# Kernel optimization log

Measured on AMD Instinct MI355X. Metric: run time of the kernel, lower is better.

Reference implementation:

```python
import jax, jax.numpy as jnp
import numpy as np

N_NODES = 50000
N_EDGES = 800000
D = 128


def _gcn_layer(x, src, dst, deg_inv_sqrt, W, b, n_nodes):
    # GCNConv: X' = D^{-1/2} (A + I) D^{-1/2} X W + b   (PyG default, self-loops added)
    h = x @ W  # [N, D]
    norm = deg_inv_sqrt[src] * deg_inv_sqrt[dst]  # [E+N]
    msgs = h[src] * norm[:, None]  # [E+N, D] gather + scale
    out = jax.ops.segment_sum(msgs, dst, num_segments=n_nodes)  # scatter-add
    return out + b


def setup_inputs() -> dict:
    key = jax.random.key(0)
    k1, k2, k3, k4 = jax.random.split(key, 4)
    x = jax.random.normal(k1, (N_NODES, D), dtype=jnp.float32)
    edge_index = jax.random.randint(k2, (2, N_EDGES), 0, N_NODES, dtype=jnp.int64)
    scale = 1.0 / np.sqrt(D)
    W1 = jax.random.normal(k3, (D, D), dtype=jnp.float32) * scale
    b1 = jnp.zeros((D,), dtype=jnp.float32)
    W2 = jax.random.normal(k4, (D, D), dtype=jnp.float32) * scale
    b2 = jnp.zeros((D,), dtype=jnp.float32)
    return {"x": x, "edge_index": edge_index, "W1": W1, "b1": b1, "W2": W2, "b2": b2}


def reference(x, edge_index, W1, b1, W2, b2):
    n_nodes = x.shape[0]
    # add self-loops once (same graph both layers)
    loop = jnp.arange(n_nodes, dtype=edge_index.dtype)
    src = jnp.concatenate([edge_index[0], loop])
    dst = jnp.concatenate([edge_index[1], loop])
    deg = jax.ops.segment_sum(jnp.ones_like(dst, dtype=x.dtype), dst, num_segments=n_nodes)
    deg_inv_sqrt = jnp.where(deg > 0, jax.lax.rsqrt(deg), 0.0)

    h = _gcn_layer(x, src, dst, deg_inv_sqrt, W1, b1, n_nodes)
    h = jax.nn.relu(h)
    h = _gcn_layer(h, src, dst, deg_inv_sqrt, W2, b2, n_nodes)
    h = jax.nn.relu(h)
    return h
```

## Files before the change

kernel.cpp:

```cpp
#include <hip/hip_runtime.h>

#define N_NODES 50000
#define N_EDGES 800000
#define D 128
#define NB 392
#define CHUNK 2048
#define NBKT 391
#define LHM (NBKT * NB)
#define NSB ((LHM + 255) / 256)
#define GB ((N_NODES + 127) / 128)

typedef unsigned int uint32;
typedef unsigned short ushort;
typedef __attribute__((ext_vector_type(8))) short s8v;
typedef __attribute__((ext_vector_type(4))) float f4v;

__device__ __forceinline__ ushort f2bf(float f) {
    unsigned u = __float_as_uint(f);
    u += 0x7FFFu + ((u >> 16) & 1u);
    return (ushort)(u >> 16);
}
__device__ __forceinline__ float bf_lo(uint32 u) { return __uint_as_float(u << 16); }
__device__ __forceinline__ float bf_hi(uint32 u) { return __uint_as_float(u & 0xFFFF0000u); }

__device__ __forceinline__ int block_incl_scan(int v, int t) {
    int lane = t & 63, wv = t >> 6;
    int incl = v;
    #pragma unroll
    for (int off = 1; off < 64; off <<= 1) {
        int u = __shfl_up(incl, off, 64);
        if (lane >= off) incl += u;
    }
    __shared__ int wsums[4];
    if (lane == 63) wsums[wv] = incl;
    __syncthreads();
    int add = 0;
    if (wv > 0) add += wsums[0];
    if (wv > 1) add += wsums[1];
    if (wv > 2) add += wsums[2];
    return incl + add;
}

__global__ __launch_bounds__(256) void phaseA_kernel(const int* __restrict__ dst,
                                                     int* __restrict__ histM,
                                                     const float* __restrict__ W1,
                                                     const float* __restrict__ W2,
                                                     ushort* __restrict__ W1t,
                                                     ushort* __restrict__ W2t) {
    int t = threadIdx.x, blk = blockIdx.x;
    if (blk >= NB) {
        const float* W = (blk - NB) ? W2 : W1;
        ushort* Wt = (blk - NB) ? W2t : W1t;
        #pragma unroll
        for (int it = 0; it < 16; it++) {
            int fid = t + it * 256;
            int k = fid >> 5;
            int n0 = (fid & 31) * 4;
            float4 w = ((const float4*)W)[fid];
            Wt[(n0 + 0) * D + k] = f2bf(w.x);
            Wt[(n0 + 1) * D + k] = f2bf(w.y);
            Wt[(n0 + 2) * D + k] = f2bf(w.z);
            Wt[(n0 + 3) * D + k] = f2bf(w.w);
        }
        return;
    }
    __shared__ int lc[NBKT];
    for (int i = t; i < NBKT; i += 256) lc[i] = 0;
    __syncthreads();
    int e0 = blk * CHUNK;
    #pragma unroll
    for (int j = 0; j < 8; j++) {
        int e = e0 + t + j * 256;
        if (e < N_EDGES) atomicAdd(&lc[dst[e] >> 7], 1);
    }
    __syncthreads();
    for (int i = t; i < NBKT; i += 256)
        histM[i * NB + blk] = lc[i];
}

__global__ __launch_bounds__(256) void scan1g(const int* __restrict__ in,
                                              int* __restrict__ out,
                                              int* __restrict__ bsum) {
    int t = threadIdx.x, blk = blockIdx.x;
    int i = blk * 256 + t;
    int v = (i < LHM) ? in[i] : 0;
    int incl = block_incl_scan(v, t);
    if (i < LHM) out[i] = incl - v;
    if (t == 255) bsum[blk] = incl;
}

__global__ __launch_bounds__(256) void scan23g(int* __restrict__ out,
                                               const int* __restrict__ bsum) {
    int t = threadIdx.x, blk = blockIdx.x;
    int local = 0;
    for (int i = t; i < blk; i += 256) local += bsum[i];
    int lane = t & 63, wv = t >> 6;
    #pragma unroll
    for (int off = 32; off > 0; off >>= 1) local += __shfl_down(local, off, 64);
    __shared__ int ws[4];
    if (lane == 0) ws[wv] = local;
    __syncthreads();
    int boff = ws[0] + ws[1] + ws[2] + ws[3];
    int i = blk * 256 + t;
    if (i < LHM) out[i] += boff;
}

__global__ __launch_bounds__(256) void phaseC_kernel(const int* __restrict__ src,
                                                     const int* __restrict__ dst,
                                                     const int* __restrict__ base,
                                                     uint32* __restrict__ edgeTmp) {
    __shared__ int cur[NBKT];
    int t = threadIdx.x, blk = blockIdx.x;
    for (int i = t; i < NBKT; i += 256) cur[i] = base[i * NB + blk];
    __syncthreads();
    int e0 = blk * CHUNK;
    #pragma unroll
    for (int j = 0; j < 8; j++) {
        int e = e0 + t + j * 256;
        if (e < N_EDGES) {
            uint32 s = (uint32)src[e], d = (uint32)dst[e];
            int p = atomicAdd(&cur[d >> 7], 1);
            edgeTmp[p] = (s << 16) | d;
        }
    }
}

__global__ __launch_bounds__(256) void phaseD_kernel(const uint32* __restrict__ edgeTmp,
                                                     const int* __restrict__ base,
                                                     int* __restrict__ rowstart,
                                                     float* __restrict__ dis,
                                                     ushort* __restrict__ e16) {
    __shared__ int cnt[128];
    __shared__ int cur[128];
    int t = threadIdx.x, b = blockIdx.x;
    int beg = base[b * NB];
    int end = (b == NBKT - 1) ? N_EDGES : base[(b + 1) * NB];
    if (t < 128) cnt[t] = 0;
    __syncthreads();
    for (int p = beg + t; p < end; p += 256)
        atomicAdd(&cnt[edgeTmp[p] & 127], 1);
    __syncthreads();
    int c = (t < 128) ? cnt[t] : 0;
    int incl = block_incl_scan(c, t);
    int excl = incl - c;
    int node = b * 128 + t;
    if (t < 128) {
        if (node <= N_NODES) rowstart[node] = beg + excl;
        if (node < N_NODES) dis[node] = rsqrtf((float)(c + 1));
        cur[t] = excl;
    }
    __syncthreads();
    for (int p = beg + t; p < end; p += 256) {
        uint32 u = edgeTmp[p];
        int r = atomicAdd(&cur[u & 127], 1);
        e16[beg + r] = (ushort)(u >> 16);
    }
}

template<bool BF16IN>
__global__ __launch_bounds__(256) void gemm_mfma(const void* __restrict__ Xv,
                                                 const ushort* __restrict__ Wt,
                                                 const float* __restrict__ dis,
                                                 ushort* __restrict__ Hb) {
    __shared__ ushort Cs[128 * 136];
    int t = threadIdx.x;
    int wv = t >> 6, lane = t & 63;
    int q = lane >> 4, m = lane & 15;
    int rbase = blockIdx.x * 128 + wv * 32;
    f4v zero = {0.f, 0.f, 0.f, 0.f};
    f4v acc[2][8];
    #pragma unroll
    for (int mt = 0; mt < 2; mt++)
        #pragma unroll
        for (int n = 0; n < 8; n++) acc[mt][n] = zero;

    #pragma unroll
    for (int kt = 0; kt < 4; kt++) {
        int k0 = kt * 32 + q * 8;
        s8v a[2];
        #pragma unroll
        for (int mt = 0; mt < 2; mt++) {
            int row = rbase + mt * 16 + m;
            if (row >= N_NODES) row = N_NODES - 1;
            if (BF16IN) {
                const ushort* xp = (const ushort*)Xv + (size_t)row * D + k0;
                a[mt] = *(const s8v*)xp;
            } else {
                const float* xp = (const float*)Xv + (size_t)row * D + k0;
                float4 u0 = *(const float4*)xp;
                float4 u1 = *(const float4*)(xp + 4);
                s8v av;
                av[0] = (short)f2bf(u0.x); av[1] = (short)f2bf(u0.y);
                av[2] = (short)f2bf(u0.z); av[3] = (short)f2bf(u0.w);
                av[4] = (short)f2bf(u1.x); av[5] = (short)f2bf(u1.y);
                av[6] = (short)f2bf(u1.z); av[7] = (short)f2bf(u1.w);
                a[mt] = av;
            }
        }
        #pragma unroll
        for (int n = 0; n < 8; n++) {
            s8v b = *(const s8v*)(Wt + (size_t)(n * 16 + m) * D + k0);
            acc[0][n] = __builtin_amdgcn_mfma_f32_16x16x32_bf16(a[0], b, acc[0][n], 0, 0, 0);
            acc[1][n] = __builtin_amdgcn_mfma_f32_16x16x32_bf16(a[1], b, acc[1][n], 0, 0, 0);
        }
    }
    float disv[2][4];
    #pragma unroll
    for (int mt = 0; mt < 2; mt++)
        #pragma unroll
        for (int r = 0; r < 4; r++) {
            int row = rbase + mt * 16 + q * 4 + r;
            if (row >= N_NODES) row = N_NODES - 1;
            disv[mt][r] = dis[row];
        }
    #pragma unroll
    for (int mt = 0; mt < 2; mt++)
        #pragma unroll
        for (int n = 0; n < 8; n++)
            #pragma unroll
            for (int r = 0; r < 4; r++) {
                int row = wv * 32 + mt * 16 + q * 4 + r;
                Cs[row * 136 + n * 16 + m] = f2bf(acc[mt][n][r] * disv[mt][r]);
            }
    __syncthreads();
    int gbase = blockIdx.x * 128;
    #pragma unroll
    for (int it = 0; it < 8; it++) {
        int cid = t + it * 256;
        int row = cid >> 4, off = (cid & 15) * 8;
        int grow = gbase + row;
        if (grow < N_NODES) {
            s8v v = *(const s8v*)(Cs + row * 136 + off);
            *(s8v*)(Hb + (size_t)grow * D + off) = v;
        }
    }
}

__device__ __forceinline__ void acc8(float* a, uint4 v) {
    a[0] += bf_lo(v.x); a[1] += bf_hi(v.x);
    a[2] += bf_lo(v.y); a[3] += bf_hi(v.y);
    a[4] += bf_lo(v.z); a[5] += bf_hi(v.z);
    a[6] += bf_lo(v.w); a[7] += bf_hi(v.w);
}

template<bool BF16OUT>
__global__ __launch_bounds__(256) void aggr_kernel(const uint4* __restrict__ Hb4,
                                                   const float* __restrict__ dis,
                                                   const int* __restrict__ rowstart,
                                                   const ushort* __restrict__ e16,
                                                   const float* __restrict__ bias,
                                                   void* __restrict__ Hout) {
    int t = threadIdx.x;
    int li = t & 15;
    int n = blockIdx.x * 16 + (t >> 4);
    float dn = dis[n];
    float a[8];
    {
        uint4 sv = Hb4[(size_t)n * 16 + li];
        a[0] = bf_lo(sv.x); a[1] = bf_hi(sv.x);
        a[2] = bf_lo(sv.y); a[3] = bf_hi(sv.y);
        a[4] = bf_lo(sv.z); a[5] = bf_hi(sv.z);
        a[6] = bf_lo(sv.w); a[7] = bf_hi(sv.w);
    }
    int beg = rowstart[n], end = rowstart[n + 1];
    int p = beg;
    for (; p + 7 < end; p += 8) {
        int s[8];
        #pragma unroll
        for (int j = 0; j < 8; j++) s[j] = e16[p + j];
        uint4 v[8];
        #pragma unroll
        for (int j = 0; j < 8; j++) v[j] = Hb4[(size_t)s[j] * 16 + li];
        #pragma unroll
        for (int j = 0; j < 8; j++) acc8(a, v[j]);
    }
    for (; p + 3 < end; p += 4) {
        int s0 = e16[p + 0], s1 = e16[p + 1], s2 = e16[p + 2], s3 = e16[p + 3];
        uint4 v0 = Hb4[(size_t)s0 * 16 + li];
        uint4 v1 = Hb4[(size_t)s1 * 16 + li];
        uint4 v2 = Hb4[(size_t)s2 * 16 + li];
        uint4 v3 = Hb4[(size_t)s3 * 16 + li];
        acc8(a, v0); acc8(a, v1); acc8(a, v2); acc8(a, v3);
    }
    for (; p < end; p++) {
        uint4 v0 = Hb4[(size_t)e16[p] * 16 + li];
        acc8(a, v0);
    }
    const float4* b4 = (const float4*)bias;
    float4 bb0 = b4[li * 2], bb1 = b4[li * 2 + 1];
    float r0 = fmaxf(fmaf(dn, a[0], bb0.x), 0.f);
    float r1 = fmaxf(fmaf(dn, a[1], bb0.y), 0.f);
    float r2 = fmaxf(fmaf(dn, a[2], bb0.z), 0.f);
    float r3 = fmaxf(fmaf(dn, a[3], bb0.w), 0.f);
    float r4 = fmaxf(fmaf(dn, a[4], bb1.x), 0.f);
    float r5 = fmaxf(fmaf(dn, a[5], bb1.y), 0.f);
    float r6 = fmaxf(fmaf(dn, a[6], bb1.z), 0.f);
    float r7 = fmaxf(fmaf(dn, a[7], bb1.w), 0.f);
    if (BF16OUT) {
        uint4 o;
        o.x = (uint32)f2bf(r0) | ((uint32)f2bf(r1) << 16);
        o.y = (uint32)f2bf(r2) | ((uint32)f2bf(r3) << 16);
        o.z = (uint32)f2bf(r4) | ((uint32)f2bf(r5) << 16);
        o.w = (uint32)f2bf(r6) | ((uint32)f2bf(r7) << 16);
        ((uint4*)Hout)[(size_t)n * 16 + li] = o;
    } else {
        float4* H4 = (float4*)Hout;
        float4 o0; o0.x = r0; o0.y = r1; o0.z = r2; o0.w = r3;
        float4 o1; o1.x = r4; o1.y = r5; o1.z = r6; o1.w = r7;
        H4[(size_t)n * 32 + li * 2]     = o0;
        H4[(size_t)n * 32 + li * 2 + 1] = o1;
    }
}

extern "C" void kernel_launch(void* const* d_in, const int* in_sizes, int n_in,
                              void* d_out, int out_size, void* d_ws, size_t ws_size,
                              hipStream_t stream) {
    const float* x  = (const float*)d_in[0];
    const int*   ei = (const int*)d_in[1];
    const float* W1 = (const float*)d_in[2];
    const float* b1 = (const float*)d_in[3];
    const float* W2 = (const float*)d_in[4];
    const float* b2 = (const float*)d_in[5];
    float* out = (float*)d_out;

    char* ws = (char*)d_ws;
    size_t off = 0;
    auto alloc = [&](size_t bytes) -> void* {
        void* p = ws + off;
        off += (bytes + 255) & ~(size_t)255;
        return p;
    };
    int*    histM    = (int*)alloc((size_t)LHM * 4);
    int*    base     = (int*)alloc((size_t)LHM * 4);
    int*    bsum     = (int*)alloc((size_t)NSB * 4);
    int*    rowstart = (int*)alloc((size_t)(N_NODES + 1) * 4);
    float*  dis      = (float*)alloc((size_t)N_NODES * 4);
    uint32* edgeTmp  = (uint32*)alloc((size_t)N_EDGES * 4);
    ushort* e16      = (ushort*)alloc((size_t)N_EDGES * 2);
    ushort* Hb       = (ushort*)alloc((size_t)N_NODES * D * 2);
    ushort* HO1      = (ushort*)alloc((size_t)N_NODES * D * 2);
    ushort* W1t      = (ushort*)alloc((size_t)D * D * 2);
    ushort* W2t      = (ushort*)alloc((size_t)D * D * 2);

    const int* src = ei;
    const int* dst = ei + N_EDGES;

    phaseA_kernel<<<NB + 2, 256, 0, stream>>>(dst, histM, W1, W2, W1t, W2t);
    scan1g<<<NSB, 256, 0, stream>>>(histM, base, bsum);
    scan23g<<<NSB, 256, 0, stream>>>(base, bsum);
    phaseC_kernel<<<NB, 256, 0, stream>>>(src, dst, base, edgeTmp);
    phaseD_kernel<<<NBKT, 256, 0, stream>>>(edgeTmp, base, rowstart, dis, e16);

    gemm_mfma<false><<<GB, 256, 0, stream>>>(x, W1t, dis, Hb);
    aggr_kernel<true><<<N_NODES / 16, 256, 0, stream>>>((const uint4*)Hb, dis, rowstart,
                                                        e16, b1, HO1);
    gemm_mfma<true><<<GB, 256, 0, stream>>>(HO1, W2t, dis, Hb);
    aggr_kernel<false><<<N_NODES / 16, 256, 0, stream>>>((const uint4*)Hb, dis, rowstart,
                                                         e16, b2, out);
}
```

Before: 204.8 us.

## Fuse first-layer GEMM into CSR finalize kernel and drop a launch

The first-layer X·W1 MFMA GEMM, including its degree-normalisation scaling, moves into the CSR-building phaseD kernel. Each 128-node bucket block computes dis in shared memory and then runs the GEMM for the same 128 rows, which removes one kernel launch and one global reread of dis. The second GEMM now writes to a separate Hb2 buffer and the aggregation grid is written as the constant PB (3125, equal to N_NODES/16). The fused kernel uses more shared memory and registers, which may lower occupancy during the edge-sorting phase.

```diff
diff --git a/kernel.cpp b/kernel.cpp
--- a/kernel.cpp
+++ b/kernel.cpp
@@ -9,6 +9,7 @@
 #define LHM (NBKT * NB)
 #define NSB ((LHM + 255) / 256)
 #define GB ((N_NODES + 127) / 128)
+#define PB 3125
 
 typedef unsigned int uint32;
 typedef unsigned short ushort;
@@ -125,13 +126,18 @@
     }
 }
 
-__global__ __launch_bounds__(256) void phaseD_kernel(const uint32* __restrict__ edgeTmp,
-                                                     const int* __restrict__ base,
-                                                     int* __restrict__ rowstart,
-                                                     float* __restrict__ dis,
-                                                     ushort* __restrict__ e16) {
+__global__ __launch_bounds__(256) void phaseDG_kernel(const uint32* __restrict__ edgeTmp,
+                                                      const int* __restrict__ base,
+                                                      int* __restrict__ rowstart,
+                                                      float* __restrict__ dis,
+                                                      ushort* __restrict__ e16,
+                                                      const float* __restrict__ X,
+                                                      const ushort* __restrict__ Wt,
+                                                      ushort* __restrict__ Hb) {
     __shared__ int cnt[128];
     __shared__ int cur[128];
+    __shared__ float disS[128];
+    __shared__ ushort Cs[128 * 136];
     int t = threadIdx.x, b = blockIdx.x;
     int beg = base[b * NB];
     int end = (b == NBKT - 1) ? N_EDGES : base[(b + 1) * NB];
@@ -146,7 +152,9 @@
     int node = b * 128 + t;
     if (t < 128) {
         if (node <= N_NODES) rowstart[node] = beg + excl;
-        if (node < N_NODES) dis[node] = rsqrtf((float)(c + 1));
+        float dv = rsqrtf((float)(c + 1));
+        if (node < N_NODES) dis[node] = dv;
+        disS[t] = dv;
         cur[t] = excl;
     }
     __syncthreads();
@@ -155,10 +163,65 @@
         int r = atomicAdd(&cur[u & 127], 1);
         e16[beg + r] = (ushort)(u >> 16);
     }
-}
-
-template<bool BF16IN>
-__global__ __launch_bounds__(256) void gemm_mfma(const void* __restrict__ Xv,
+    int wv = t >> 6, lane = t & 63;
+    int q = lane >> 4, m = lane & 15;
+    int rbase = b * 128 + wv * 32;
+    f4v zero = {0.f, 0.f, 0.f, 0.f};
+    f4v acc[2][8];
+    #pragma unroll
+    for (int mt = 0; mt < 2; mt++)
+        #pragma unroll
+        for (int n = 0; n < 8; n++) acc[mt][n] = zero;
+    #pragma unroll
+    for (int kt = 0; kt < 4; kt++) {
+        int k0 = kt * 32 + q * 8;
+        s8v a[2];
+        #pragma unroll
+        for (int mt = 0; mt < 2; mt++) {
+            int row = rbase + mt * 16 + m;
+            if (row >= N_NODES) row = N_NODES - 1;
+            const float* xp = X + (size_t)row * D + k0;
+            float4 u0 = *(const float4*)xp;
+            float4 u1 = *(const float4*)(xp + 4);
+            s8v av;
+            av[0] = (short)f2bf(u0.x); av[1] = (short)f2bf(u0.y);
+            av[2] = (short)f2bf(u0.z); av[3] = (short)f2bf(u0.w);
+            av[4] = (short)f2bf(u1.x); av[5] = (short)f2bf(u1.y);
+            av[6] = (short)f2bf(u1.z); av[7] = (short)f2bf(u1.w);
+            a[mt] = av;
+        }
+        #pragma unroll
+        for (int n = 0; n < 8; n++) {
+            s8v bb = *(const s8v*)(Wt + (size_t)(n * 16 + m) * D + k0);
+            acc[0][n] = __builtin_amdgcn_mfma_f32_16x16x32_bf16(a[0], bb, acc[0][n], 0, 0, 0);
+            acc[1][n] = __builtin_amdgcn_mfma_f32_16x16x32_bf16(a[1], bb, acc[1][n], 0, 0, 0);
+        }
+    }
+    __syncthreads();
+    #pragma unroll
+    for (int mt = 0; mt < 2; mt++)
+        #pragma unroll
+        for (int n = 0; n < 8; n++)
+            #pragma unroll
+            for (int r = 0; r < 4; r++) {
+                int lr = wv * 32 + mt * 16 + q * 4 + r;
+                Cs[lr * 136 + n * 16 + m] = f2bf(acc[mt][n][r] * disS[lr]);
+            }
+    __syncthreads();
+    int gbase = b * 128;
+    #pragma unroll
+    for (int it = 0; it < 8; it++) {
+        int cid = t + it * 256;
+        int row = cid >> 4, off = (cid & 15) * 8;
+        int grow = gbase + row;
+        if (grow < N_NODES) {
+            s8v v = *(const s8v*)(Cs + row * 136 + off);
+            *(s8v*)(Hb + (size_t)grow * D + off) = v;
+        }
+    }
+}
+
+__global__ __launch_bounds__(256) void gemm_mfma(const ushort* __restrict__ Xb,
                                                  const ushort* __restrict__ Wt,
                                                  const float* __restrict__ dis,
                                                  ushort* __restrict__ Hb) {
@@ -182,20 +245,7 @@
         for (int mt = 0; mt < 2; mt++) {
             int row = rbase + mt * 16 + m;
             if (row >= N_NODES) row = N_NODES - 1;
-            if (BF16IN) {
-                const ushort* xp = (const ushort*)Xv + (size_t)row * D + k0;
-                a[mt] = *(const s8v*)xp;
-            } else {
-                const float* xp = (const float*)Xv + (size_t)row * D + k0;
-                float4 u0 = *(const float4*)xp;
-                float4 u1 = *(const float4*)(xp + 4);
-                s8v av;
-                av[0] = (short)f2bf(u0.x); av[1] = (short)f2bf(u0.y);
-                av[2] = (short)f2bf(u0.z); av[3] = (short)f2bf(u0.w);
-                av[4] = (short)f2bf(u1.x); av[5] = (short)f2bf(u1.y);
-                av[6] = (short)f2bf(u1.z); av[7] = (short)f2bf(u1.w);
-                a[mt] = av;
-            }
+            a[mt] = *(const s8v*)(Xb + (size_t)row * D + k0);
         }
         #pragma unroll
         for (int n = 0; n < 8; n++) {
@@ -339,6 +389,7 @@
     ushort* e16      = (ushort*)alloc((size_t)N_EDGES * 2);
     ushort* Hb       = (ushort*)alloc((size_t)N_NODES * D * 2);
     ushort* HO1      = (ushort*)alloc((size_t)N_NODES * D * 2);
+    ushort* Hb2      = (ushort*)alloc((size_t)N_NODES * D * 2);
     ushort* W1t      = (ushort*)alloc((size_t)D * D * 2);
     ushort* W2t      = (ushort*)alloc((size_t)D * D * 2);
 
@@ -349,12 +400,11 @@
     scan1g<<<NSB, 256, 0, stream>>>(histM, base, bsum);
     scan23g<<<NSB, 256, 0, stream>>>(base, bsum);
     phaseC_kernel<<<NB, 256, 0, stream>>>(src, dst, base, edgeTmp);
-    phaseD_kernel<<<NBKT, 256, 0, stream>>>(edgeTmp, base, rowstart, dis, e16);
-
-    gemm_mfma<false><<<GB, 256, 0, stream>>>(x, W1t, dis, Hb);
-    aggr_kernel<true><<<N_NODES / 16, 256, 0, stream>>>((const uint4*)Hb, dis, rowstart,
-                                                        e16, b1, HO1);
-    gemm_mfma<true><<<GB, 256, 0, stream>>>(HO1, W2t, dis, Hb);
-    aggr_kernel<false><<<N_NODES / 16, 256, 0, stream>>>((const uint4*)Hb, dis, rowstart,
-                                                         e16, b2, out);
-}
+    phaseDG_kernel<<<NBKT, 256, 0, stream>>>(edgeTmp, base, rowstart, dis, e16,
+                                             x, W1t, Hb);
+    aggr_kernel<true><<<PB, 256, 0, stream>>>((const uint4*)Hb, dis, rowstart,
+                                              e16, b1, HO1);
+    gemm_mfma<<<GB, 256, 0, stream>>>(HO1, W2t, dis, Hb2);
+    aggr_kernel<false><<<PB, 256, 0, stream>>>((const uint4*)Hb2, dis, rowstart,
+                                               e16, b2, out);
+}
```

Result: no change. 202.3 us (-1.2%).
